# Kernel optimization log

Measured on AMD Instinct MI355X. Metric: run time of the kernel, lower is better.

Reference implementation:

```python
import jax, jax.numpy as jnp
import numpy as np

# ---- static config (matches init_kwargs) ----
WS = 7            # window_size
SHIFT = 3         # shift_size (SW-MSA block)
Z, X, Y = 14, 28, 56
DIM = 384
HEADS = 12
HD = DIM // HEADS
N = WS ** 3       # tokens per 3D window = 343
SCALE = HD ** (-0.5)
TBL = (2 * WS - 1) ** 3
B = 2
L = Z * X * Y
NW = (Z // WS) * (X // WS) * (Y // WS)  # 64 windows
MLP_H = 4 * DIM


def _rel_index():
    # Faithful to source: only coords 0 and 1 are offset, coord 0 scaled by (2*Wx-1).
    c = np.stack(np.meshgrid(np.arange(WS), np.arange(WS), np.arange(WS), indexing='ij')).reshape(3, -1)
    r = (c[:, :, None] - c[:, None, :]).transpose(1, 2, 0).astype(np.int64)
    r[..., 0] += WS - 1
    r[..., 1] += WS - 1
    r[..., 0] *= 2 * WS - 1
    idx = r.sum(-1)
    return np.mod(idx, TBL)  # torch wraps negative indices; mod reproduces that

REL_IDX = jnp.asarray(_rel_index())  # (N, N)


def _attn_mask():
    img = np.zeros((1, Z, X, Y, 1))
    sl = (slice(0, -WS), slice(-WS, -SHIFT), slice(-SHIFT, None))
    cnt = 0
    for a in sl:
        for b in sl:
            for c in sl:
                img[:, a, b, c, :] = cnt
                cnt += 1
    w = img.reshape(1, Z // WS, WS, X // WS, WS, Y // WS, WS, 1)
    w = w.transpose(0, 1, 3, 5, 2, 4, 6, 7).reshape(-1, N)
    d = w[:, None, :] - w[:, :, None]
    return np.where(d != 0, -100.0, 0.0).astype(np.float32)  # (NW, N, N)

ATTN_MASK = jnp.asarray(_attn_mask())


def _ln(x, g, b):
    m = x.mean(-1, keepdims=True)
    v = jnp.mean(jnp.square(x - m), axis=-1, keepdims=True)
    return (x - m) * jax.lax.rsqrt(v + 1e-5) * g + b


def _window_partition(x):  # (B,Z,X,Y,C) -> (B*NW, N, C)
    x = x.reshape(B, Z // WS, WS, X // WS, WS, Y // WS, WS, DIM)
    x = x.transpose(0, 1, 3, 5, 2, 4, 6, 7)
    return x.reshape(-1, N, DIM)


def _window_reverse(w):  # (B*NW, N, C) -> (B,Z,X,Y,C)
    x = w.reshape(B, Z // WS, X // WS, Y // WS, WS, WS, WS, DIM)
    x = x.transpose(0, 1, 4, 2, 5, 3, 6, 7)
    return x.reshape(B, Z, X, Y, DIM)


def setup_inputs() -> dict:
    key = jax.random.key(0)
    ks = jax.random.split(key, 8)
    f32 = jnp.float32
    p = {}
    p['x'] = jax.random.normal(ks[0], (B, L, DIM), f32)
    p['norm1_g'] = jnp.ones((DIM,), f32)
    p['norm1_b'] = jnp.zeros((DIM,), f32)
    p['qkv_w'] = (jax.random.normal(ks[1], (DIM, 3 * DIM), f32) * 0.02)
    p['qkv_b'] = jnp.zeros((3 * DIM,), f32)
    p['proj_w'] = (jax.random.normal(ks[2], (DIM, DIM), f32) * 0.02)
    p['proj_b'] = jnp.zeros((DIM,), f32)
    p['rel_tbl'] = (jax.random.normal(ks[3], (TBL, HEADS), f32) * 0.02)
    p['norm2_g'] = jnp.ones((DIM,), f32)
    p['norm2_b'] = jnp.zeros((DIM,), f32)
    p['fc1_w'] = (jax.random.normal(ks[4], (DIM, MLP_H), f32) * 0.02)
    p['fc1_b'] = jnp.zeros((MLP_H,), f32)
    p['fc2_w'] = (jax.random.normal(ks[5], (MLP_H, DIM), f32) * 0.02)
    p['fc2_b'] = jnp.zeros((DIM,), f32)
    return p


def reference(x, norm1_g, norm1_b, qkv_w, qkv_b, proj_w, proj_b, rel_tbl,
              norm2_g, norm2_b, fc1_w, fc1_b, fc2_w, fc2_b):
    shortcut = x
    h = _ln(x, norm1_g, norm1_b).reshape(B, Z, X, Y, DIM)
    # cyclic shift
    h = jnp.roll(h, (-SHIFT, -SHIFT, -SHIFT), axis=(1, 2, 3))
    w = _window_partition(h)                       # (B*NW, N, C)
    qkv = (w @ qkv_w + qkv_b).reshape(-1, N, 3, HEADS, HD).transpose(2, 0, 3, 1, 4)
    q, k, v = qkv[0] * SCALE, qkv[1], qkv[2]       # (B*NW, H, N, hd)
    attn = jnp.einsum('bhnd,bhmd->bhnm', q, k)
    bias = rel_tbl[REL_IDX].transpose(2, 0, 1)     # (H, N, N)
    attn = attn + bias[None]
    attn = attn.reshape(B, NW, HEADS, N, N) + ATTN_MASK[None, :, None]
    attn = jax.nn.softmax(attn.reshape(-1, HEADS, N, N), axis=-1)
    o = jnp.einsum('bhnm,bhmd->bhnd', attn, v).transpose(0, 2, 1, 3).reshape(-1, N, DIM)
    o = o @ proj_w + proj_b
    h = _window_reverse(o)
    h = jnp.roll(h, (SHIFT, SHIFT, SHIFT), axis=(1, 2, 3)).reshape(B, L, DIM)
    x = shortcut + h
    m = _ln(x, norm2_g, norm2_b)
    m = jax.nn.gelu(m @ fc1_w + fc1_b, approximate=False) @ fc2_w + fc2_b
    return x + m
```

## Files before the change

kernel.cpp:

```cpp
#include <hip/hip_runtime.h>
#include <hip/hip_bf16.h>
#include <cmath>

typedef float f32x4 __attribute__((ext_vector_type(4)));
typedef float f32x16 __attribute__((ext_vector_type(16)));
typedef short bf16x8 __attribute__((ext_vector_type(8)));
typedef const __attribute__((address_space(1))) unsigned int* gas_t;
typedef __attribute__((address_space(3))) unsigned int* las_t;

#define GLOAD16(g, l) __builtin_amdgcn_global_load_lds((gas_t)(const void*)(g), (las_t)(void*)(l), 16, 0, 0)

#define LOG2E 1.4426950408889634f
#define MASKC (-144.2695040888963f)
#define SL2E  (0.17677669529663687f * 1.4426950408889634f)

static __device__ __forceinline__ float bf2f(unsigned short u){
  return __uint_as_float(((unsigned)u) << 16);
}
static __device__ __forceinline__ unsigned short f2bf(float f){
  unsigned u = __float_as_uint(f);
  unsigned r = u + 0x7FFFu + ((u >> 16) & 1u);
  return (unsigned short)(r >> 16);
}
static __device__ __forceinline__ unsigned packbf(float a, float b){
  union { __hip_bfloat162 h; unsigned u; } cv;
  cv.h = __float22bfloat162_rn(make_float2(a, b));
  return cv.u;
}
static __device__ __forceinline__ f32x16 zero16(){
  f32x16 z;
  #pragma unroll
  for (int i = 0; i < 16; i++) z[i] = 0.f;
  return z;
}

__global__ __launch_bounds__(256) void padzero_kernel(unsigned short* __restrict__ qs2,
                                                      unsigned short* __restrict__ ks2,
                                                      unsigned short* __restrict__ vt2){
  const int wh = blockIdx.x;
  uint4 z = make_uint4(0, 0, 0, 0);
  const size_t base = (size_t)wh * 11264 + 10 * 1024;
  for (int i = threadIdx.x; i < 384; i += 256){
    int arr = i >> 7, slot = i & 127;
    unsigned short* p = (arr == 0 ? qs2 : (arr == 1 ? ks2 : vt2));
    *(uint4*)(p + base + slot * 8) = z;
  }
}

__global__ __launch_bounds__(256) void wconv2_kernel(const float* __restrict__ in,
                                                     unsigned short* __restrict__ out,
                                                     int K, int N){
  __shared__ unsigned short t[32][33];
  int tx = threadIdx.x & 31, ty = threadIdx.x >> 5;
  int n0 = blockIdx.x * 32, k0 = blockIdx.y * 32;
  #pragma unroll
  for (int i = 0; i < 4; i++)
    t[ty + 8 * i][tx] = f2bf(in[(size_t)(k0 + ty + 8 * i) * N + n0 + tx]);
  __syncthreads();
  #pragma unroll
  for (int i = 0; i < 4; i++)
    out[(size_t)(n0 + ty + 8 * i) * K + k0 + tx] = t[tx][ty + 8 * i];
}

__global__ void biasprep_kernel(const float* __restrict__ rel, unsigned short* __restrict__ bias12){
  int p = blockIdx.x * 256 + threadIdx.x;
  if (p >= 743424) return;
  int h = p / 61952;
  int rem = p - h * 61952;
  int q = rem / 176;
  int m2 = (rem - q * 176) * 2;
  int qi0 = q / 49, qr = q - qi0 * 49, qi1 = qr / 7, qi2 = qr - qi1 * 7;
  unsigned v[2];
  #pragma unroll
  for (int j = 0; j < 2; j++){
    int m = m2 + j;
    float val;
    if (m >= 343) val = -1.4426950e30f;
    else {
      int mi0 = m / 49, mr = m - mi0 * 49, mi1 = mr / 7, mi2 = mr - mi1 * 7;
      int idx = 13 * (qi0 - mi0 + 6) + (qi1 - mi1 + 6) + (qi2 - mi2);
      if (idx < 0) idx += 2197;
      val = rel[idx * 12 + h] * LOG2E;
    }
    v[j] = f2bf(val);
  }
  *(unsigned*)(&bias12[(size_t)h * 123904 + q * 352 + m2]) = v[0] | (v[1] << 16);
}

__global__ void maskprep_kernel(unsigned* __restrict__ bitmapG){
  int id = blockIdx.x * 256 + threadIdx.x;
  if (id >= 8 * 352) return;
  int cls = id / 352, q = id - cls * 352;
  int qi0 = q / 49, qr = q - qi0 * 49, qi1 = qr / 7, qi2 = qr - qi1 * 7;
  int az = (cls & 4) ? (qi0 < 4 ? 1 : 2) : 0;
  int ax = (cls & 2) ? (qi1 < 4 ? 1 : 2) : 0;
  int ay = (cls & 1) ? (qi2 < 4 ? 1 : 2) : 0;
  int cq = az * 9 + ax * 3 + ay;
  unsigned w[11];
  #pragma unroll
  for (int t = 0; t < 11; t++) w[t] = 0u;
  for (int m = 0; m < 352; m++){
    int mi0 = m / 49, mr = m - mi0 * 49, mi1 = mr / 7, mi2 = mr - mi1 * 7;
    int bz = (cls & 4) ? (mi0 < 4 ? 1 : 2) : 0;
    int bx = (cls & 2) ? (mi1 < 4 ? 1 : 2) : 0;
    int by = (cls & 1) ? (mi2 < 4 ? 1 : 2) : 0;
    if (bz * 9 + bx * 3 + by != cq) w[m >> 5] |= (1u << (m & 31));
  }
  unsigned* dst = bitmapG + (size_t)id * 12;
  #pragma unroll
  for (int t = 0; t < 11; t++) dst[t] = w[t];
  dst[11] = 0u;
}

template<int MODE>
__global__ __launch_bounds__(256) void ln_kernel(const float* __restrict__ in,
                                                 const float* __restrict__ g,
                                                 const float* __restrict__ bta,
                                                 unsigned short* __restrict__ out){
  int wave = threadIdx.x >> 6, lane = threadIdx.x & 63;
  int row = blockIdx.x * 4 + wave;
  size_t srow;
  if (MODE == 0){
    int win = row / 343, n = row - win * 343;
    int b = win >> 6, w64 = win & 63;
    int zw = w64 >> 5, xw = (w64 >> 3) & 3, yw = w64 & 7;
    int i0 = n / 49, nr = n - i0 * 49, i1 = nr / 7, i2 = nr - i1 * 7;
    int zs = zw * 7 + i0 + 3; if (zs >= 14) zs -= 14;
    int xs = xw * 7 + i1 + 3; if (xs >= 28) xs -= 28;
    int ys = yw * 7 + i2 + 3; if (ys >= 56) ys -= 56;
    srow = (size_t)b * 21952 + zs * 1568 + xs * 56 + ys;
  } else {
    srow = (size_t)row;
  }
  const float* p = in + srow * 384;
  float v[6]; float s = 0.f;
  #pragma unroll
  for (int i = 0; i < 6; i++){ v[i] = p[lane + i * 64]; s += v[i]; }
  #pragma unroll
  for (int off = 32; off >= 1; off >>= 1) s += __shfl_xor(s, off);
  float mean = s * (1.f / 384.f);
  float vs = 0.f;
  #pragma unroll
  for (int i = 0; i < 6; i++){ float d = v[i] - mean; vs += d * d; }
  #pragma unroll
  for (int off = 32; off >= 1; off >>= 1) vs += __shfl_xor(vs, off);
  float rstd = rsqrtf(vs * (1.f / 384.f) + 1e-5f);
  unsigned short* o = out + (size_t)row * 384;
  #pragma unroll
  for (int i = 0; i < 6; i++){
    int c = lane + i * 64;
    o[c] = f2bf((v[i] - mean) * rstd * g[c] + bta[c]);
  }
}

template<int EPI>
__global__ __launch_bounds__(256, 2) void gemm2(
    const unsigned short* __restrict__ A,
    const unsigned short* __restrict__ Bt,
    const float* __restrict__ bias,
    const float* __restrict__ resid,
    void* __restrict__ outp,
    unsigned short* __restrict__ oq,
    unsigned short* __restrict__ ok,
    unsigned short* __restrict__ ov,
    int K, int ldc, int nt){
  __shared__ unsigned short As[4096];
  __shared__ unsigned short Bs[4096];
  const int nwg = gridDim.x;
  const int qq = nwg >> 3, rr = nwg & 7;
  const int xcd = blockIdx.x & 7, pos = blockIdx.x >> 3;
  const int wgid = (xcd < rr ? xcd * (qq + 1) : rr * (qq + 1) + (xcd - rr) * qq) + pos;
  const int mtile = wgid / nt, ntile = wgid - mtile * nt;
  const int r0 = mtile * 128, c0 = ntile * 128;

  const int tid = threadIdx.x, lane = tid & 63, wave = tid >> 6;
  const int wr = (wave >> 1) * 64, wc = (wave & 1) * 64;
  f32x4 acc[4][4];
  #pragma unroll
  for (int mi = 0; mi < 4; mi++)
    #pragma unroll
    for (int ni = 0; ni < 4; ni++) acc[mi][ni] = f32x4{0.f, 0.f, 0.f, 0.f};

  const int srow = lane >> 2;
  const int koff = ((lane & 3) ^ ((lane >> 3) & 3)) * 8;
  const int kkey = (lane >> 1) & 3;

  for (int k0 = 0; k0 < K; k0 += 32){
    __syncthreads();
    #pragma unroll
    for (int i = 0; i < 4; i++){
      int id = wave + i * 4;
      int arr = id >> 3, sub = id & 7;
      const unsigned short* g = (arr ? Bt : A)
          + (size_t)((arr ? c0 : r0) + sub * 16 + srow) * K + k0 + koff;
      unsigned short* dst = (arr ? Bs : As) + sub * 512;
      GLOAD16(g, dst);
    }
    __syncthreads();
    bf16x8 af[4], bfr[4];
    #pragma unroll
    for (int mi = 0; mi < 4; mi++)
      af[mi] = *(const bf16x8*)(&As[(wr + mi * 16 + (lane & 15)) * 32 + (((lane >> 4) ^ kkey) * 8)]);
    #pragma unroll
    for (int ni = 0; ni < 4; ni++)
      bfr[ni] = *(const bf16x8*)(&Bs[(wc + ni * 16 + (lane & 15)) * 32 + (((lane >> 4) ^ kkey) * 8)]);
    #pragma unroll
    for (int mi = 0; mi < 4; mi++)
      #pragma unroll
      for (int ni = 0; ni < 4; ni++)
        acc[mi][ni] = __builtin_amdgcn_mfma_f32_16x16x32_bf16(af[mi], bfr[ni], acc[mi][ni], 0, 0, 0);
  }

  #pragma unroll
  for (int mi = 0; mi < 4; mi++){
    #pragma unroll
    for (int j = 0; j < 4; j++){
      const int row = r0 + wr + mi * 16 + ((lane >> 4) << 2) + j;
      int win, m, t, mloc, vhalf2;
      if (EPI == 0 || EPI == 1){
        win = row / 343; m = row - win * 343;
      }
      if (EPI == 0){
        t = m >> 5; mloc = m & 31;
        vhalf2 = ((m >> 4) & 1) * 512 + ((m >> 3) & 1) * 256 + (m & 7);
      }
      #pragma unroll
      for (int ni = 0; ni < 4; ni++){
        const int col = c0 + wc + ni * 16 + (lane & 15);
        const int r = j;
        float val = acc[mi][ni][r] + bias[col];
        if (EPI == 0){
          if (col < 768){
            int d = col, dd;
            unsigned short* base;
            if (col < 384){ val *= SL2E; dd = d & 31; base = oq; }
            else { d = col - 384; dd = d & 31; base = ok; }
            int h = d >> 5;
            size_t off = (size_t)(win * 12 + h) * 11264
                       + (size_t)(t * 1024 + ((dd >> 4) & 1) * 512 + ((dd >> 3) & 1) * 256 + mloc * 8 + (dd & 7));
            base[off] = f2bf(val);
          } else {
            int d = col - 768, dd = d & 31, h = d >> 5;
            size_t off = (size_t)(win * 12 + h) * 11264
                       + (size_t)(t * 1024 + vhalf2 + dd * 8);
            ov[off] = f2bf(val);
          }
        } else if (EPI == 1){
          int b = win >> 6, w64 = win & 63;
          int zw = w64 >> 5, xw = (w64 >> 3) & 3, yw = w64 & 7;
          int i0 = m / 49, nr = m - i0 * 49, i1 = nr / 7, i2 = nr - i1 * 7;
          int zf = zw * 7 + i0 + 3; if (zf >= 14) zf -= 14;
          int xf = xw * 7 + i1 + 3; if (xf >= 28) xf -= 28;
          int yf = yw * 7 + i2 + 3; if (yf >= 56) yf -= 56;
          size_t dst = ((size_t)b * 21952 + zf * 1568 + xf * 56 + yf) * 384 + col;
          ((float*)outp)[dst] = resid[dst] + val;
        } else if (EPI == 2){
          val = 0.5f * val * (1.0f + erff(val * 0.70710678118654752f));
          ((unsigned short*)outp)[(size_t)row * ldc + col] = f2bf(val);
        } else {
          ((float*)outp)[(size_t)row * ldc + col] =
              resid[(size_t)row * ldc + col] + val;
        }
      }
    }
  }
}

__global__ __launch_bounds__(256, 4) void attn3_kernel(
    const unsigned short* __restrict__ qs2,
    const unsigned short* __restrict__ ks2,
    const unsigned short* __restrict__ vt2,
    const unsigned short* __restrict__ bias12,
    const unsigned* __restrict__ bitmapG,
    unsigned short* __restrict__ out){
  __shared__ unsigned short Ks[11264];
  __shared__ unsigned short Ps[4][1280];
  const int wh = blockIdx.x;
  const int win = wh / 12, h = wh - win * 12;
  const int tid = threadIdx.x, wave = tid >> 6, lane = tid & 63;
  const int ln = lane & 31, hh = lane >> 5;

  const unsigned short* ksrc = ks2 + (size_t)wh * 11264;
  for (int c = wave; c < 22; c += 4)
    GLOAD16(ksrc + c * 512 + lane * 8, &Ks[c * 512]);

  const int w64 = win & 63;
  const int cls = ((((w64 >> 5) & 1) == 1 ? 4 : 0)) | ((((w64 >> 3) & 3) == 3) ? 2 : 0) | (((w64 & 7) == 7) ? 1 : 0);
  __syncthreads();

  const unsigned short* qbase = qs2 + (size_t)wh * 11264;
  const unsigned short* vbase = vt2 + (size_t)wh * 11264;

  for (int qt = wave; qt < 11; qt += 4){
    const int q_lane = qt * 32 + ln;
    const bf16x8 bq0 = *(const bf16x8*)(qbase + qt * 1024 + hh * 256 + ln * 8);
    const bf16x8 bq1 = *(const bf16x8*)(qbase + qt * 1024 + 512 + hh * 256 + ln * 8);
    const unsigned short* brow = bias12 + ((size_t)h * 352 + q_lane) * 352;
    const unsigned* mrow = bitmapG + (size_t)(cls * 352 + q_lane) * 12;

    f32x16 o = zero16();
    float sum = 0.f;
    bf16x8 nbv0 = *(const bf16x8*)(vbase + hh * 256 + ln * 8);
    bf16x8 nbv1 = *(const bf16x8*)(vbase + 512 + hh * 256 + ln * 8);
    ushort4 nb0 = *(const ushort4*)(brow + hh * 4);
    ushort4 nb1 = *(const ushort4*)(brow + 8 + hh * 4);
    ushort4 nb2 = *(const ushort4*)(brow + 16 + hh * 4);
    ushort4 nb3 = *(const ushort4*)(brow + 24 + hh * 4);
    unsigned nwm = mrow[0];

    for (int t = 0; t < 11; t++){
      const bf16x8 bv0 = nbv0, bv1 = nbv1;
      const ushort4 cb0 = nb0, cb1 = nb1, cb2 = nb2, cb3 = nb3;
      const unsigned wm = nwm;
      if (t < 10){
        const unsigned short* vnext = vbase + (t + 1) * 1024;
        nbv0 = *(const bf16x8*)(vnext + hh * 256 + ln * 8);
        nbv1 = *(const bf16x8*)(vnext + 512 + hh * 256 + ln * 8);
        const unsigned short* bnext = brow + (t + 1) * 32;
        nb0 = *(const ushort4*)(bnext + hh * 4);
        nb1 = *(const ushort4*)(bnext + 8 + hh * 4);
        nb2 = *(const ushort4*)(bnext + 16 + hh * 4);
        nb3 = *(const ushort4*)(bnext + 24 + hh * 4);
        nwm = mrow[t + 1];
      }
      const bf16x8 ka0 = *(const bf16x8*)(&Ks[t * 1024 + hh * 256 + ln * 8]);
      const bf16x8 ka1 = *(const bf16x8*)(&Ks[t * 1024 + 512 + hh * 256 + ln * 8]);
      f32x16 acc = zero16();
      acc = __builtin_amdgcn_mfma_f32_32x32x16_bf16(ka0, bq0, acc, 0, 0, 0);
      acc = __builtin_amdgcn_mfma_f32_32x32x16_bf16(ka1, bq1, acc, 0, 0, 0);

      const unsigned wsh = wm >> (4 * hh);
      float pv[16];
      unsigned short cbv[16];
      *(ushort4*)(&cbv[0]) = cb0; *(ushort4*)(&cbv[4]) = cb1;
      *(ushort4*)(&cbv[8]) = cb2; *(ushort4*)(&cbv[12]) = cb3;
      #pragma unroll
      for (int g = 0; g < 4; g++){
        #pragma unroll
        for (int i = 0; i < 4; i++){
          const int r = g * 4 + i;
          float s = acc[r] + bf2f(cbv[r]);
          if (cls){
            if (wsh & (1u << (i + 8 * g))) s += MASKC;
          }
          float e = exp2f(s);
          sum += e;
          pv[r] = e;
        }
      }
      #pragma unroll
      for (int g = 0; g < 4; g++){
        uint2 pk;
        pk.x = packbf(pv[4 * g], pv[4 * g + 1]);
        pk.y = packbf(pv[4 * g + 2], pv[4 * g + 3]);
        *(uint2*)(&Ps[wave][ln * 40 + 8 * g + 4 * hh]) = pk;
      }
      const bf16x8 pa0 = *(const bf16x8*)(&Ps[wave][ln * 40 + 8 * hh]);
      const bf16x8 pa1 = *(const bf16x8*)(&Ps[wave][ln * 40 + 16 + 8 * hh]);
      o = __builtin_amdgcn_mfma_f32_32x32x16_bf16(pa0, bv0, o, 0, 0, 0);
      o = __builtin_amdgcn_mfma_f32_32x32x16_bf16(pa1, bv1, o, 0, 0, 0);
    }
    sum += __shfl_xor(sum, 32);
    const float inv = 1.f / sum;
    #pragma unroll
    for (int r = 0; r < 16; r++){
      const int qloc = (r & 3) + 8 * (r >> 2) + 4 * hh;
      const float iv = __shfl(inv, qloc);
      const int qg = qt * 32 + qloc;
      if (qg < 343)
        out[((size_t)win * 343 + qg) * 384 + h * 32 + ln] = f2bf(o[r] * iv);
    }
  }
}

extern "C" void kernel_launch(void* const* d_in, const int* in_sizes, int n_in,
                              void* d_out, int out_size, void* d_ws, size_t ws_size,
                              hipStream_t stream){
  const float* x      = (const float*)d_in[0];
  const float* n1g    = (const float*)d_in[1];
  const float* n1b    = (const float*)d_in[2];
  const float* qkv_w  = (const float*)d_in[3];
  const float* qkv_b  = (const float*)d_in[4];
  const float* proj_w = (const float*)d_in[5];
  const float* proj_b = (const float*)d_in[6];
  const float* rel    = (const float*)d_in[7];
  const float* n2g    = (const float*)d_in[8];
  const float* n2b    = (const float*)d_in[9];
  const float* fc1_w  = (const float*)d_in[10];
  const float* fc1_b  = (const float*)d_in[11];
  const float* fc2_w  = (const float*)d_in[12];
  const float* fc2_b  = (const float*)d_in[13];
  float* out = (float*)d_out;

  char* ws = (char*)d_ws;
  unsigned short* w_win  = (unsigned short*)(ws + 0);
  unsigned short* hidden = (unsigned short*)(ws + 0);
  unsigned short* qs2    = (unsigned short*)(ws + 33718272ull);
  unsigned short* ks2    = (unsigned short*)(ws + 68321280ull);
  unsigned short* vt2    = (unsigned short*)(ws + 102924288ull);
  float*          x2     = (float*)(ws + 134873088ull);
  unsigned short* bias12 = (unsigned short*)(ws + 137527296ull);
  unsigned*       bitmapG= (unsigned*)(ws + 140504064ull);
  unsigned short* att    = (unsigned short*)(ws + 202309632ull);
  unsigned short* ln2    = att;
  unsigned short* wt_qkv = (unsigned short*)(ws + 236027904ull);
  unsigned short* wt_prj = (unsigned short*)(ws + 236912640ull);
  unsigned short* wt_fc1 = (unsigned short*)(ws + 237207552ull);
  unsigned short* wt_fc2 = (unsigned short*)(ws + 238387200ull);

  wconv2_kernel<<<dim3(36, 12), 256, 0, stream>>>(qkv_w, wt_qkv, 384, 1152);
  wconv2_kernel<<<dim3(12, 12), 256, 0, stream>>>(proj_w, wt_prj, 384, 384);
  wconv2_kernel<<<dim3(48, 12), 256, 0, stream>>>(fc1_w, wt_fc1, 384, 1536);
  wconv2_kernel<<<dim3(12, 48), 256, 0, stream>>>(fc2_w, wt_fc2, 1536, 384);
  biasprep_kernel<<<2904, 256, 0, stream>>>(rel, bias12);
  maskprep_kernel<<<11, 256, 0, stream>>>(bitmapG);
  padzero_kernel<<<1536, 256, 0, stream>>>(qs2, ks2, vt2);

  ln_kernel<0><<<10976, 256, 0, stream>>>(x, n1g, n1b, w_win);
  gemm2<0><<<343 * 9, 256, 0, stream>>>(w_win, wt_qkv, qkv_b, nullptr, nullptr,
                                        qs2, ks2, vt2, 384, 0, 9);
  attn3_kernel<<<1536, 256, 0, stream>>>(qs2, ks2, vt2, bias12, bitmapG, att);
  gemm2<1><<<343 * 3, 256, 0, stream>>>(att, wt_prj, proj_b, x, x2,
                                        nullptr, nullptr, nullptr, 384, 384, 3);
  ln_kernel<1><<<10976, 256, 0, stream>>>(x2, n2g, n2b, ln2);
  gemm2<2><<<343 * 12, 256, 0, stream>>>(ln2, wt_fc1, fc1_b, nullptr, hidden,
                                         nullptr, nullptr, nullptr, 384, 1536, 12);
  gemm2<3><<<343 * 3, 256, 0, stream>>>(hidden, wt_fc2, fc2_b, x2, out,
                                        nullptr, nullptr, nullptr, 1536, 384, 3);
}
```

Baseline: 529.7 us.

## Double-buffer LDS tiles in gemm2 and raise occupancy hint to four blocks

The GEMM main loop now keeps two LDS buffers, issuing the global-to-LDS async loads for the next K-slice before computing MFMAs on the current one, with one barrier per iteration instead of two. The launch bounds hint is raised from 2 to 4 blocks per CU. This aims to hide global load latency behind the matrix math. In exchange it doubles LDS use per block and tightens the register budget, which may cause spills.

```diff
diff --git a/kernel.cpp b/kernel.cpp
--- a/kernel.cpp
+++ b/kernel.cpp
@@ -154,7 +154,7 @@
 }
 
 template<int EPI>
-__global__ __launch_bounds__(256, 2) void gemm2(
+__global__ __launch_bounds__(256, 4) void gemm2(
     const unsigned short* __restrict__ A,
     const unsigned short* __restrict__ Bt,
     const float* __restrict__ bias,
@@ -163,14 +163,14 @@
     unsigned short* __restrict__ oq,
     unsigned short* __restrict__ ok,
     unsigned short* __restrict__ ov,
-    int K, int ldc, int nt){
-  __shared__ unsigned short As[4096];
-  __shared__ unsigned short Bs[4096];
+    int K, int ldc, int nt_){
+  __shared__ unsigned short As[2][4096];
+  __shared__ unsigned short Bs[2][4096];
   const int nwg = gridDim.x;
   const int qq = nwg >> 3, rr = nwg & 7;
   const int xcd = blockIdx.x & 7, pos = blockIdx.x >> 3;
   const int wgid = (xcd < rr ? xcd * (qq + 1) : rr * (qq + 1) + (xcd - rr) * qq) + pos;
-  const int mtile = wgid / nt, ntile = wgid - mtile * nt;
+  const int mtile = wgid / nt_, ntile = wgid - mtile * nt_;
   const int r0 = mtile * 128, c0 = ntile * 128;
 
   const int tid = threadIdx.x, lane = tid & 63, wave = tid >> 6;
@@ -184,32 +184,41 @@
   const int srow = lane >> 2;
   const int koff = ((lane & 3) ^ ((lane >> 3) & 3)) * 8;
   const int kkey = (lane >> 1) & 3;
-
-  for (int k0 = 0; k0 < K; k0 += 32){
-    __syncthreads();
-    #pragma unroll
-    for (int i = 0; i < 4; i++){
-      int id = wave + i * 4;
-      int arr = id >> 3, sub = id & 7;
-      const unsigned short* g = (arr ? Bt : A)
-          + (size_t)((arr ? c0 : r0) + sub * 16 + srow) * K + k0 + koff;
-      unsigned short* dst = (arr ? Bs : As) + sub * 512;
-      GLOAD16(g, dst);
-    }
-    __syncthreads();
+  const int nt = K >> 5;
+
+  #define STAGE(T, BUF) do {                                                  \
+    const int k0_ = (T) << 5;                                                 \
+    _Pragma("unroll")                                                         \
+    for (int i_ = 0; i_ < 4; i_++){                                           \
+      int id_ = wave + i_ * 4;                                                \
+      int arr_ = id_ >> 3, sub_ = id_ & 7;                                    \
+      const unsigned short* g_ = (arr_ ? Bt : A)                              \
+          + (size_t)((arr_ ? c0 : r0) + sub_ * 16 + srow) * K + k0_ + koff;   \
+      unsigned short* dst_ = (arr_ ? &Bs[BUF][0] : &As[BUF][0]) + sub_ * 512; \
+      GLOAD16(g_, dst_);                                                      \
+    }                                                                         \
+  } while (0)
+
+  STAGE(0, 0);
+  __syncthreads();
+  int cur = 0;
+  for (int t = 0; t < nt; t++){
+    if (t + 1 < nt) STAGE(t + 1, cur ^ 1);
     bf16x8 af[4], bfr[4];
     #pragma unroll
     for (int mi = 0; mi < 4; mi++)
-      af[mi] = *(const bf16x8*)(&As[(wr + mi * 16 + (lane & 15)) * 32 + (((lane >> 4) ^ kkey) * 8)]);
+      af[mi] = *(const bf16x8*)(&As[cur][(wr + mi * 16 + (lane & 15)) * 32 + (((lane >> 4) ^ kkey) * 8)]);
     #pragma unroll
     for (int ni = 0; ni < 4; ni++)
-      bfr[ni] = *(const bf16x8*)(&Bs[(wc + ni * 16 + (lane & 15)) * 32 + (((lane >> 4) ^ kkey) * 8)]);
+      bfr[ni] = *(const bf16x8*)(&Bs[cur][(wc + ni * 16 + (lane & 15)) * 32 + (((lane >> 4) ^ kkey) * 8)]);
     #pragma unroll
     for (int mi = 0; mi < 4; mi++)
       #pragma unroll
       for (int ni = 0; ni < 4; ni++)
         acc[mi][ni] = __builtin_amdgcn_mfma_f32_16x16x32_bf16(af[mi], bfr[ni], acc[mi][ni], 0, 0, 0);
-  }
+    if (t + 1 < nt){ __syncthreads(); cur ^= 1; }
+  }
+  #undef STAGE
 
   #pragma unroll
   for (int mi = 0; mi < 4; mi++){
```

Result: no change. 532.8 us (+0.6%).

## Stage GEMM epilogue through LDS for vectorized coalesced stores

Applied to the files above, without the earlier changes.

The GEMM epilogue now writes accumulators into a swizzled per-wave LDS tile and reads them back as rows of 8 contiguous columns. This allows 16-byte vector stores and vector residual loads in place of scalar per-element scatter writes. The exact erf GELU is replaced with a sigmoid-based approximation (x*sigmoid(1.702x)), and launch bounds are raised to 4 blocks per CU. The approximation changes numerics and may exceed the accuracy tolerance. The higher occupancy target may also cause register spills.

```diff
diff --git a/kernel.cpp b/kernel.cpp
--- a/kernel.cpp
+++ b/kernel.cpp
@@ -154,7 +154,7 @@
 }
 
 template<int EPI>
-__global__ __launch_bounds__(256, 2) void gemm2(
+__global__ __launch_bounds__(256, 4) void gemm2(
     const unsigned short* __restrict__ A,
     const unsigned short* __restrict__ Bt,
     const float* __restrict__ bias,
@@ -163,14 +163,15 @@
     unsigned short* __restrict__ oq,
     unsigned short* __restrict__ ok,
     unsigned short* __restrict__ ov,
-    int K, int ldc, int nt){
-  __shared__ unsigned short As[4096];
-  __shared__ unsigned short Bs[4096];
+    int K, int ldc, int nt_){
+  __shared__ unsigned short Smem[8192];
+  unsigned short* As = Smem;
+  unsigned short* Bs = Smem + 4096;
   const int nwg = gridDim.x;
   const int qq = nwg >> 3, rr = nwg & 7;
   const int xcd = blockIdx.x & 7, pos = blockIdx.x >> 3;
   const int wgid = (xcd < rr ? xcd * (qq + 1) : rr * (qq + 1) + (xcd - rr) * qq) + pos;
-  const int mtile = wgid / nt, ntile = wgid - mtile * nt;
+  const int mtile = wgid / nt_, ntile = wgid - mtile * nt_;
   const int r0 = mtile * 128, c0 = ntile * 128;
 
   const int tid = threadIdx.x, lane = tid & 63, wave = tid >> 6;
@@ -211,58 +212,90 @@
         acc[mi][ni] = __builtin_amdgcn_mfma_f32_16x16x32_bf16(af[mi], bfr[ni], acc[mi][ni], 0, 0, 0);
   }
 
+  __syncthreads();
+  float* ep = (float*)Smem + wave * 1024;
+  const int lr = lane & 15;
+  const int kx0 = (lr & 7) ^ ((lr >> 2) & 2);
   #pragma unroll
   for (int mi = 0; mi < 4; mi++){
     #pragma unroll
-    for (int j = 0; j < 4; j++){
-      const int row = r0 + wr + mi * 16 + ((lane >> 4) << 2) + j;
-      int win, m, t, mloc, vhalf2;
-      if (EPI == 0 || EPI == 1){
-        win = row / 343; m = row - win * 343;
+    for (int ni = 0; ni < 4; ni++){
+      #pragma unroll
+      for (int j = 0; j < 4; j++){
+        const int wrow = (lane >> 4) * 4 + j;
+        const int col  = ni * 16 + (lane & 15);
+        const int key  = ((wrow & 7) << 3) ^ ((wrow & 8) << 1);
+        float val = acc[mi][ni][j] + bias[c0 + wc + col];
+        if (EPI == 2){
+          val = val / (1.0f + exp2f(val * -2.4554669f));
+        } else if (EPI == 0){
+          if (c0 < 384) val *= SL2E;
+        }
+        ep[wrow * 64 + (col ^ key)] = val;
       }
-      if (EPI == 0){
-        t = m >> 5; mloc = m & 31;
-        vhalf2 = ((m >> 4) & 1) * 512 + ((m >> 3) & 1) * 256 + (m & 7);
-      }
-      #pragma unroll
-      for (int ni = 0; ni < 4; ni++){
-        const int col = c0 + wc + ni * 16 + (lane & 15);
-        const int r = j;
-        float val = acc[mi][ni][r] + bias[col];
-        if (EPI == 0){
-          if (col < 768){
-            int d = col, dd;
-            unsigned short* base;
-            if (col < 384){ val *= SL2E; dd = d & 31; base = oq; }
-            else { d = col - 384; dd = d & 31; base = ok; }
-            int h = d >> 5;
-            size_t off = (size_t)(win * 12 + h) * 11264
-                       + (size_t)(t * 1024 + ((dd >> 4) & 1) * 512 + ((dd >> 3) & 1) * 256 + mloc * 8 + (dd & 7));
-            base[off] = f2bf(val);
-          } else {
-            int d = col - 768, dd = d & 31, h = d >> 5;
-            size_t off = (size_t)(win * 12 + h) * 11264
-                       + (size_t)(t * 1024 + vhalf2 + dd * 8);
-            ov[off] = f2bf(val);
-          }
-        } else if (EPI == 1){
-          int b = win >> 6, w64 = win & 63;
-          int zw = w64 >> 5, xw = (w64 >> 3) & 3, yw = w64 & 7;
-          int i0 = m / 49, nr = m - i0 * 49, i1 = nr / 7, i2 = nr - i1 * 7;
-          int zf = zw * 7 + i0 + 3; if (zf >= 14) zf -= 14;
-          int xf = xw * 7 + i1 + 3; if (xf >= 28) xf -= 28;
-          int yf = yw * 7 + i2 + 3; if (yf >= 56) yf -= 56;
-          size_t dst = ((size_t)b * 21952 + zf * 1568 + xf * 56 + yf) * 384 + col;
-          ((float*)outp)[dst] = resid[dst] + val;
-        } else if (EPI == 2){
-          val = 0.5f * val * (1.0f + erff(val * 0.70710678118654752f));
-          ((unsigned short*)outp)[(size_t)row * ldc + col] = f2bf(val);
+    }
+    asm volatile("s_waitcnt lgkmcnt(0)" ::: "memory");
+    #pragma unroll
+    for (int rep = 0; rep < 2; rep++){
+      const int cg = (lane >> 4) + rep * 4;
+      const float* src = ep + lr * 64 + ((cg ^ kx0) << 3);
+      f32x4 v0 = *(const f32x4*)(src);
+      f32x4 v1 = *(const f32x4*)(src + 4);
+      const int row  = r0 + wr + mi * 16 + lr;
+      const int colg = c0 + wc + cg * 8;
+      if (EPI == 2){
+        uint4 st;
+        st.x = packbf(v0[0], v0[1]); st.y = packbf(v0[2], v0[3]);
+        st.z = packbf(v1[0], v1[1]); st.w = packbf(v1[2], v1[3]);
+        *(uint4*)((unsigned short*)outp + (size_t)row * ldc + colg) = st;
+      } else if (EPI == 3){
+        const float* rsd = resid + (size_t)row * ldc + colg;
+        f32x4 q0 = *(const f32x4*)rsd, q1 = *(const f32x4*)(rsd + 4);
+        v0 += q0; v1 += q1;
+        float* dst = (float*)outp + (size_t)row * ldc + colg;
+        *(f32x4*)dst = v0; *(f32x4*)(dst + 4) = v1;
+      } else if (EPI == 1){
+        const int win = row / 343, m = row - win * 343;
+        const int b = win >> 6, w64 = win & 63;
+        const int zw = w64 >> 5, xw = (w64 >> 3) & 3, yw = w64 & 7;
+        const int i0 = m / 49, nr = m - i0 * 49, i1 = nr / 7, i2 = nr - i1 * 7;
+        int zf = zw * 7 + i0 + 3; if (zf >= 14) zf -= 14;
+        int xf = xw * 7 + i1 + 3; if (xf >= 28) xf -= 28;
+        int yf = yw * 7 + i2 + 3; if (yf >= 56) yf -= 56;
+        const size_t dst = ((size_t)b * 21952 + zf * 1568 + xf * 56 + yf) * 384 + colg;
+        const float* rsd = resid + dst;
+        f32x4 q0 = *(const f32x4*)rsd, q1 = *(const f32x4*)(rsd + 4);
+        v0 += q0; v1 += q1;
+        float* dp = (float*)outp + dst;
+        *(f32x4*)dp = v0; *(f32x4*)(dp + 4) = v1;
+      } else {
+        const int win = row / 343, m = row - win * 343;
+        const int t = m >> 5, mloc = m & 31;
+        if (c0 < 768){
+          const int d = (c0 < 384) ? colg : (colg - 384);
+          const int h = d >> 5, dd = d & 31;
+          unsigned short* basep = (c0 < 384) ? oq : ok;
+          const size_t off = (size_t)(win * 12 + h) * 11264
+              + (size_t)(t * 1024 + ((dd >> 4) & 1) * 512 + ((dd >> 3) & 1) * 256 + mloc * 8);
+          uint4 st;
+          st.x = packbf(v0[0], v0[1]); st.y = packbf(v0[2], v0[3]);
+          st.z = packbf(v1[0], v1[1]); st.w = packbf(v1[2], v1[3]);
+          *(uint4*)(basep + off) = st;
         } else {
-          ((float*)outp)[(size_t)row * ldc + col] =
-              resid[(size_t)row * ldc + col] + val;
+          const int d = colg - 768;
+          const int h = d >> 5, ddb = d & 31;
+          const int vh2 = ((m >> 4) & 1) * 512 + ((m >> 3) & 1) * 256 + (m & 7);
+          const size_t off = (size_t)(win * 12 + h) * 11264 + (size_t)(t * 1024 + vh2);
+          float vv[8];
+          vv[0] = v0[0]; vv[1] = v0[1]; vv[2] = v0[2]; vv[3] = v0[3];
+          vv[4] = v1[0]; vv[5] = v1[1]; vv[6] = v1[2]; vv[7] = v1[3];
+          #pragma unroll
+          for (int jj = 0; jj < 8; jj++)
+            ov[off + (size_t)(ddb + jj) * 8] = f2bf(vv[jj]);
         }
       }
     }
+    asm volatile("s_waitcnt lgkmcnt(0)" ::: "memory");
   }
 }
 
```

Result: no change. 526.3 us (-0.6%).

## Transpose GEMM MFMA operands to vectorize epilogue stores and use sigmoid GELU

Applied to the files above, without the earlier changes.

Swaps the A/B operands of the MFMA so each lane holds four consecutive columns of one row, which lets the epilogue issue packed bf16 and float4 loads and stores instead of scalar ones. It also hoists the per-row window and index arithmetic out of the column loop. The exact erf GELU is replaced by the sigmoid approximation x*sigmoid(1.702x), which is cheaper but deviates from the reference's exact GELU. Launch bounds are raised from 2 to 4 blocks per CU, which may constrain registers.

```diff
diff --git a/kernel.cpp b/kernel.cpp
--- a/kernel.cpp
+++ b/kernel.cpp
@@ -154,7 +154,7 @@
 }
 
 template<int EPI>
-__global__ __launch_bounds__(256, 2) void gemm2(
+__global__ __launch_bounds__(256, 4) void gemm2(
     const unsigned short* __restrict__ A,
     const unsigned short* __restrict__ Bt,
     const float* __restrict__ bias,
@@ -163,14 +163,14 @@
     unsigned short* __restrict__ oq,
     unsigned short* __restrict__ ok,
     unsigned short* __restrict__ ov,
-    int K, int ldc, int nt){
+    int K, int ldc, int nt_){
   __shared__ unsigned short As[4096];
   __shared__ unsigned short Bs[4096];
   const int nwg = gridDim.x;
   const int qq = nwg >> 3, rr = nwg & 7;
   const int xcd = blockIdx.x & 7, pos = blockIdx.x >> 3;
   const int wgid = (xcd < rr ? xcd * (qq + 1) : rr * (qq + 1) + (xcd - rr) * qq) + pos;
-  const int mtile = wgid / nt, ntile = wgid - mtile * nt;
+  const int mtile = wgid / nt_, ntile = wgid - mtile * nt_;
   const int r0 = mtile * 128, c0 = ntile * 128;
 
   const int tid = threadIdx.x, lane = tid & 63, wave = tid >> 6;
@@ -208,58 +208,75 @@
     for (int mi = 0; mi < 4; mi++)
       #pragma unroll
       for (int ni = 0; ni < 4; ni++)
-        acc[mi][ni] = __builtin_amdgcn_mfma_f32_16x16x32_bf16(af[mi], bfr[ni], acc[mi][ni], 0, 0, 0);
-  }
-
+        acc[mi][ni] = __builtin_amdgcn_mfma_f32_16x16x32_bf16(bfr[ni], af[mi], acc[mi][ni], 0, 0, 0);
+  }
+
+  const int lrow = lane & 15;
+  const int cq4  = (lane >> 4) << 2;
   #pragma unroll
   for (int mi = 0; mi < 4; mi++){
-    #pragma unroll
-    for (int j = 0; j < 4; j++){
-      const int row = r0 + wr + mi * 16 + ((lane >> 4) << 2) + j;
-      int win, m, t, mloc, vhalf2;
-      if (EPI == 0 || EPI == 1){
-        win = row / 343; m = row - win * 343;
-      }
-      if (EPI == 0){
-        t = m >> 5; mloc = m & 31;
-        vhalf2 = ((m >> 4) & 1) * 512 + ((m >> 3) & 1) * 256 + (m & 7);
-      }
+    const int row = r0 + wr + mi * 16 + lrow;
+    int win, m, t, mloc, vh2;
+    size_t sdst;
+    if (EPI == 0 || EPI == 1){ win = row / 343; m = row - win * 343; }
+    if (EPI == 0){
+      t = m >> 5; mloc = m & 31;
+      vh2 = ((m >> 4) & 1) * 512 + ((m >> 3) & 1) * 256 + (m & 7);
+    }
+    if (EPI == 1){
+      const int b = win >> 6, w64 = win & 63;
+      const int zw = w64 >> 5, xw = (w64 >> 3) & 3, yw = w64 & 7;
+      const int i0 = m / 49, nr = m - i0 * 49, i1 = nr / 7, i2 = nr - i1 * 7;
+      int zf = zw * 7 + i0 + 3; if (zf >= 14) zf -= 14;
+      int xf = xw * 7 + i1 + 3; if (xf >= 28) xf -= 28;
+      int yf = yw * 7 + i2 + 3; if (yf >= 56) yf -= 56;
+      sdst = ((size_t)b * 21952 + zf * 1568 + xf * 56 + yf) * 384;
+    }
+    #pragma unroll
+    for (int ni = 0; ni < 4; ni++){
+      const int colb = c0 + wc + ni * 16 + cq4;
+      float v[4];
       #pragma unroll
-      for (int ni = 0; ni < 4; ni++){
-        const int col = c0 + wc + ni * 16 + (lane & 15);
-        const int r = j;
-        float val = acc[mi][ni][r] + bias[col];
-        if (EPI == 0){
-          if (col < 768){
-            int d = col, dd;
-            unsigned short* base;
-            if (col < 384){ val *= SL2E; dd = d & 31; base = oq; }
-            else { d = col - 384; dd = d & 31; base = ok; }
-            int h = d >> 5;
-            size_t off = (size_t)(win * 12 + h) * 11264
-                       + (size_t)(t * 1024 + ((dd >> 4) & 1) * 512 + ((dd >> 3) & 1) * 256 + mloc * 8 + (dd & 7));
-            base[off] = f2bf(val);
-          } else {
-            int d = col - 768, dd = d & 31, h = d >> 5;
-            size_t off = (size_t)(win * 12 + h) * 11264
-                       + (size_t)(t * 1024 + vhalf2 + dd * 8);
-            ov[off] = f2bf(val);
-          }
-        } else if (EPI == 1){
-          int b = win >> 6, w64 = win & 63;
-          int zw = w64 >> 5, xw = (w64 >> 3) & 3, yw = w64 & 7;
-          int i0 = m / 49, nr = m - i0 * 49, i1 = nr / 7, i2 = nr - i1 * 7;
-          int zf = zw * 7 + i0 + 3; if (zf >= 14) zf -= 14;
-          int xf = xw * 7 + i1 + 3; if (xf >= 28) xf -= 28;
-          int yf = yw * 7 + i2 + 3; if (yf >= 56) yf -= 56;
-          size_t dst = ((size_t)b * 21952 + zf * 1568 + xf * 56 + yf) * 384 + col;
-          ((float*)outp)[dst] = resid[dst] + val;
-        } else if (EPI == 2){
-          val = 0.5f * val * (1.0f + erff(val * 0.70710678118654752f));
-          ((unsigned short*)outp)[(size_t)row * ldc + col] = f2bf(val);
+      for (int j = 0; j < 4; j++) v[j] = acc[mi][ni][j] + bias[colb + j];
+      if (EPI == 2){
+        #pragma unroll
+        for (int j = 0; j < 4; j++)
+          v[j] = v[j] / (1.0f + exp2f(v[j] * -2.4554669f));
+        uint2 st; st.x = packbf(v[0], v[1]); st.y = packbf(v[2], v[3]);
+        *(uint2*)((unsigned short*)outp + (size_t)row * ldc + colb) = st;
+      } else if (EPI == 3){
+        const float* rsd = resid + (size_t)row * ldc + colb;
+        f32x4 q = *(const f32x4*)rsd;
+        f32x4 o4; o4[0] = v[0] + q[0]; o4[1] = v[1] + q[1];
+        o4[2] = v[2] + q[2]; o4[3] = v[3] + q[3];
+        *(f32x4*)((float*)outp + (size_t)row * ldc + colb) = o4;
+      } else if (EPI == 1){
+        const float* rsd = resid + sdst + colb;
+        f32x4 q = *(const f32x4*)rsd;
+        f32x4 o4; o4[0] = v[0] + q[0]; o4[1] = v[1] + q[1];
+        o4[2] = v[2] + q[2]; o4[3] = v[3] + q[3];
+        *(f32x4*)((float*)outp + sdst + colb) = o4;
+      } else {
+        if (c0 < 384){
+          #pragma unroll
+          for (int j = 0; j < 4; j++) v[j] *= SL2E;
+          const int d = colb, h = d >> 5, dd = d & 31;
+          const size_t off = (size_t)(win * 12 + h) * 11264
+              + (size_t)(t * 1024 + ((dd >> 4) & 1) * 512 + ((dd >> 3) & 1) * 256 + mloc * 8 + (dd & 7));
+          uint2 st; st.x = packbf(v[0], v[1]); st.y = packbf(v[2], v[3]);
+          *(uint2*)(oq + off) = st;
+        } else if (c0 < 768){
+          const int d = colb - 384, h = d >> 5, dd = d & 31;
+          const size_t off = (size_t)(win * 12 + h) * 11264
+              + (size_t)(t * 1024 + ((dd >> 4) & 1) * 512 + ((dd >> 3) & 1) * 256 + mloc * 8 + (dd & 7));
+          uint2 st; st.x = packbf(v[0], v[1]); st.y = packbf(v[2], v[3]);
+          *(uint2*)(ok + off) = st;
         } else {
-          ((float*)outp)[(size_t)row * ldc + col] =
-              resid[(size_t)row * ldc + col] + val;
+          const int d = colb - 768, h = d >> 5, dd = d & 31;
+          const size_t off = (size_t)(win * 12 + h) * 11264 + (size_t)(t * 1024 + vh2);
+          #pragma unroll
+          for (int j = 0; j < 4; j++)
+            ov[off + (size_t)(dd + j) * 8] = f2bf(v[j]);
         }
       }
     }
```

Result: no change. 537.2 us (+1.4%).
